# Kernel optimization log

Measured on AMD Instinct MI355X. Metric: run time of the kernel, lower is better.

## Reference

```python
import jax, jax.numpy as jnp
import numpy as np

HIDDEN = 1024
HEADS = 16
HEAD_DIM = HIDDEN // HEADS


def setup_inputs() -> dict:
    key = jax.random.key(0)
    ks = jax.random.split(key, 9)
    B, S, D = 8, 1370, HIDDEN
    x = jax.random.normal(ks[0], (B, S, D), dtype=jnp.float32)
    s = 1.0 / np.sqrt(D)
    Wq = jax.random.normal(ks[1], (D, D), dtype=jnp.float32) * s
    bq = jnp.zeros((D,), dtype=jnp.float32)
    Wk = jax.random.normal(ks[2], (D, D), dtype=jnp.float32) * s
    bk = jnp.zeros((D,), dtype=jnp.float32)
    Wv = jax.random.normal(ks[3], (D, D), dtype=jnp.float32) * s
    bv = jnp.zeros((D,), dtype=jnp.float32)
    Wo = jax.random.normal(ks[4], (D, D), dtype=jnp.float32) * s
    bo = jnp.zeros((D,), dtype=jnp.float32)
    return {"x": x, "Wq": Wq, "bq": bq, "Wk": Wk, "bk": bk,
            "Wv": Wv, "bv": bv, "Wo": Wo, "bo": bo}


def reference(x, Wq, bq, Wk, bk, Wv, bv, Wo, bo):
    B, S, D = x.shape
    H, Dh = HEADS, HEAD_DIM
    # separate Q/K/V projections
    q = (x @ Wq + bq).reshape(B, S, H, Dh).transpose(0, 2, 1, 3)  # [B,H,S,Dh]
    k = (x @ Wk + bk).reshape(B, S, H, Dh).transpose(0, 2, 1, 3)
    v = (x @ Wv + bv).reshape(B, S, H, Dh).transpose(0, 2, 1, 3)
    scale = jnp.asarray(Dh, q.dtype) ** -0.5
    attn = jnp.einsum('bhqd,bhkd->bhqk', q, k) * scale  # [B,H,S,S]
    attn = jax.nn.softmax(attn, axis=-1)
    out = jnp.einsum('bhqk,bhkd->bhqd', attn, v)        # [B,H,S,Dh]
    out = out.transpose(0, 2, 1, 3).reshape(B, S, D)
    return out @ Wo + bo
```

## Files before the change

### kernel.cpp

```cpp
#include <hip/hip_runtime.h>
#include <stdint.h>

#define DEV __device__ __forceinline__

typedef unsigned short u16;
typedef __attribute__((ext_vector_type(8))) __bf16 bf16x8;
typedef __attribute__((ext_vector_type(8))) u16 u16x8;
typedef __attribute__((ext_vector_type(4))) u16 u16x4;
typedef __attribute__((ext_vector_type(4))) float floatx4;

#define S_LEN 1370
#define S_PAD 1408
#define NH 16
#define DH 64
#define M_TOK (8 * S_LEN)
#define NKT (S_PAD / 64)
#define CEXP 0.18033688f

DEV u16 f2bf(float f) {
    union { float f; uint32_t u; } v; v.f = f;
    uint32_t u = v.u + 0x7fffu + ((v.u >> 16) & 1u);
    return (u16)(u >> 16);
}

typedef const __attribute__((address_space(1))) void as1_cvoid;
typedef __attribute__((address_space(3))) void as3_void;

DEV void async16(const void* g, void* s) {
    __builtin_amdgcn_global_load_lds((as1_cvoid*)g, (as3_void*)s, 16, 0, 0);
}

__global__ void cvt_bf16(const float* __restrict__ src, u16* __restrict__ dst) {
    const size_t i0 = ((size_t)blockIdx.x * 256 + threadIdx.x) * 8;
    const float4 a = *(const float4*)(src + i0);
    const float4 b = *(const float4*)(src + i0 + 4);
    u16x8 o;
    o[0] = f2bf(a.x); o[1] = f2bf(a.y); o[2] = f2bf(a.z); o[3] = f2bf(a.w);
    o[4] = f2bf(b.x); o[5] = f2bf(b.y); o[6] = f2bf(b.z); o[7] = f2bf(b.w);
    *(u16x8*)(dst + i0) = o;
}

__global__ void transpose4(const float* __restrict__ w0, const float* __restrict__ w1,
                           const float* __restrict__ w2, const float* __restrict__ w3,
                           u16* __restrict__ t0, u16* __restrict__ t1,
                           u16* __restrict__ t2, u16* __restrict__ t3) {
    __shared__ u16 tile[64][65];
    const float* src; u16* dst;
    switch (blockIdx.z) {
        case 0: src = w0; dst = t0; break;
        case 1: src = w1; dst = t1; break;
        case 2: src = w2; dst = t2; break;
        default: src = w3; dst = t3; break;
    }
    const int tx = blockIdx.x, ty = blockIdx.y, tid = threadIdx.x;
#pragma unroll
    for (int i = 0; i < 16; i++) {
        int e = i * 256 + tid, r = e >> 6, c = e & 63;
        tile[r][c] = f2bf(src[(size_t)(ty * 64 + r) * 1024 + tx * 64 + c]);
    }
    __syncthreads();
#pragma unroll
    for (int i = 0; i < 16; i++) {
        int e = i * 256 + tid, r = e >> 6, c = e & 63;
        dst[(size_t)(tx * 64 + r) * 1024 + ty * 64 + c] = tile[c][r];
    }
}

#define GEMM_KLOOP(M_, N_)                                                     \
    floatx4 acc[4][4];                                                         \
    _Pragma("unroll")                                                          \
    for (int i = 0; i < 4; i++)                                                \
        _Pragma("unroll")                                                      \
        for (int j = 0; j < 4; j++) acc[i][j] = (floatx4){0.f, 0.f, 0.f, 0.f}; \
    const int srow = tid >> 2;                                                 \
    const int kb = (tid & 3) * 16;                                             \
    int ar0 = mbase + srow;          if (ar0 > (M_) - 1) ar0 = (M_) - 1;       \
    int ar1 = mbase + 64 + srow;     if (ar1 > (M_) - 1) ar1 = (M_) - 1;       \
    int br0 = nbase + srow;          if (br0 > (N_) - 1) br0 = (N_) - 1;       \
    int br1 = nbase + 64 + srow;     if (br1 > (N_) - 1) br1 = (N_) - 1;       \
    const char* pA = (const char*)A;                                           \
    const char* pB = (const char*)BT;                                          \
    char* ldsA = (char*)As + w * 1024;                                         \
    char* ldsB = (char*)Bs + w * 1024;                                         \
    for (int kt = 0; kt < 32; kt++) {                                          \
        const int koff = kt * 64 + kb;                                         \
        async16(pA + (size_t)ar0 * 2048 + koff, ldsA);                         \
        async16(pA + (size_t)ar1 * 2048 + koff, ldsA + 4096);                  \
        async16(pB + (size_t)br0 * 2048 + koff, ldsB);                         \
        async16(pB + (size_t)br1 * 2048 + koff, ldsB + 4096);                  \
        __syncthreads();                                                       \
        bf16x8 af[4], bfv[4];                                                  \
        _Pragma("unroll")                                                      \
        for (int mi = 0; mi < 4; mi++)                                         \
            af[mi] = __builtin_bit_cast(bf16x8,                                \
                *(const u16x8*)&As[(wm + mi * 16 + l15) * 32 + quad * 8]);     \
        _Pragma("unroll")                                                      \
        for (int ni = 0; ni < 4; ni++)                                         \
            bfv[ni] = __builtin_bit_cast(bf16x8,                               \
                *(const u16x8*)&Bs[(wn + ni * 16 + l15) * 32 + quad * 8]);     \
        _Pragma("unroll")                                                      \
        for (int mi = 0; mi < 4; mi++)                                         \
            _Pragma("unroll")                                                  \
            for (int ni = 0; ni < 4; ni++)                                     \
                acc[mi][ni] = __builtin_amdgcn_mfma_f32_16x16x32_bf16(         \
                    af[mi], bfv[ni], acc[mi][ni], 0, 0, 0);                    \
        __syncthreads();                                                       \
    }

__global__ void gemm_qkv(const u16* __restrict__ A, const u16* __restrict__ BT,
                         const float* __restrict__ bq, const float* __restrict__ bk,
                         const float* __restrict__ bv, u16* __restrict__ Cq,
                         u16* __restrict__ Ck, u16* __restrict__ VT, int M) {
    __shared__ u16 As[128 * 32];
    __shared__ u16 Bs[128 * 32];
    const int tid = threadIdx.x;
    const int w = tid >> 6, lane = tid & 63, quad = lane >> 4, l15 = lane & 15;
    const int mbase = blockIdx.x * 128, nbase = blockIdx.y * 128;
    const int wm = (w >> 1) * 64, wn = (w & 1) * 64;

    GEMM_KLOOP(M, 3072)

    const int sel = nbase >> 10;
    if (sel == 0) {
#pragma unroll
        for (int ni = 0; ni < 4; ni++) {
            const int n = nbase + wn + ni * 16 + l15;
            const float bb = bq[n];
#pragma unroll
            for (int mi = 0; mi < 4; mi++)
#pragma unroll
                for (int r = 0; r < 4; r++) {
                    const int m = mbase + wm + mi * 16 + quad * 4 + r;
                    if (m < M) Cq[(size_t)m * 1024 + n] = f2bf((acc[mi][ni][r] + bb) * CEXP);
                }
        }
    } else if (sel == 1) {
#pragma unroll
        for (int ni = 0; ni < 4; ni++) {
            const int n = nbase - 1024 + wn + ni * 16 + l15;
            const float bb = bk[n];
#pragma unroll
            for (int mi = 0; mi < 4; mi++)
#pragma unroll
                for (int r = 0; r < 4; r++) {
                    const int m = mbase + wm + mi * 16 + quad * 4 + r;
                    if (m < M) Ck[(size_t)m * 1024 + n] = f2bf(acc[mi][ni][r] + bb);
                }
        }
    } else {
#pragma unroll
        for (int ni = 0; ni < 4; ni++) {
            const int fe = nbase - 2048 + wn + ni * 16 + l15;
            const float bb = bv[fe];
            const int hh = fe >> 6, dd = fe & 63;
#pragma unroll
            for (int mi = 0; mi < 4; mi++)
#pragma unroll
                for (int r = 0; r < 4; r++) {
                    const int m = mbase + wm + mi * 16 + quad * 4 + r;
                    if (m < M) {
                        const int btk = m / S_LEN;
                        const int ss = m - btk * S_LEN;
                        VT[(size_t)((btk * NH + hh) * DH + dd) * S_PAD + ss] =
                            f2bf(acc[mi][ni][r] + bb);
                    }
                }
        }
    }
}

__global__ void gemm_o(const u16* __restrict__ A, const u16* __restrict__ BT,
                       const float* __restrict__ bias, float* __restrict__ C, int M) {
    __shared__ u16 As[128 * 32];
    __shared__ u16 Bs[128 * 32];
    const int tid = threadIdx.x;
    const int w = tid >> 6, lane = tid & 63, quad = lane >> 4, l15 = lane & 15;
    const int mbase = blockIdx.x * 128, nbase = blockIdx.y * 128;
    const int wm = (w >> 1) * 64, wn = (w & 1) * 64;

    GEMM_KLOOP(M, 1024)

#pragma unroll
    for (int ni = 0; ni < 4; ni++) {
        const int n = nbase + wn + ni * 16 + l15;
        const float bb = bias[n];
#pragma unroll
        for (int mi = 0; mi < 4; mi++)
#pragma unroll
            for (int r = 0; r < 4; r++) {
                const int m = mbase + wm + mi * 16 + quad * 4 + r;
                if (m < M) C[(size_t)m * 1024 + n] = acc[mi][ni][r] + bb;
            }
    }
}

__global__ void flash_attn(const u16* __restrict__ Q, const u16* __restrict__ K,
                           const u16* __restrict__ VT, u16* __restrict__ O) {
    __shared__ u16 Ks[2 * 64 * 32];
    __shared__ u16 Vs[2 * 64 * 32];
    __shared__ u16 Ps[4][32 * 72];

    const int tid = threadIdx.x;
    const int w = tid >> 6, lane = tid & 63, quad = lane >> 4, l15 = lane & 15;
    const int bh = blockIdx.x, b = bh >> 4, h = bh & 15;
    const int q0 = blockIdx.y * 128 + w * 32;

    bf16x8 qf[2][2];
#pragma unroll
    for (int mi = 0; mi < 2; mi++) {
        int qr = q0 + mi * 16 + l15;
        if (qr > S_LEN - 1) qr = S_LEN - 1;
        const u16* qp = Q + (size_t)(b * S_LEN + qr) * 1024 + h * 64 + quad * 8;
        qf[mi][0] = __builtin_bit_cast(bf16x8, *(const u16x8*)qp);
        qf[mi][1] = __builtin_bit_cast(bf16x8, *(const u16x8*)(qp + 32));
    }

    floatx4 o_acc[2][4];
#pragma unroll
    for (int mi = 0; mi < 2; mi++)
#pragma unroll
        for (int nd = 0; nd < 4; nd++) o_acc[mi][nd] = (floatx4){0.f, 0.f, 0.f, 0.f};
    float lacc[2] = {0.f, 0.f};

    const int lrow = lane >> 2;
    const int scol = ((lane & 3) ^ ((lane >> 3) & 3)) * 16;
    const char* Kbl = (const char*)K + ((size_t)b * S_LEN * 1024 + h * 64) * 2 + scol;
    const char* Vbl = (const char*)VT +
                      ((size_t)(bh * 64 + w * 16 + lrow) * S_PAD) * 2 + scol;
    char* KsB = (char*)Ks;
    char* VsB = (char*)Vs;
    u16* Pw = Ps[w];

    const int rcol = (quad ^ ((l15 >> 1) & 3)) * 16;

#define STAGE(KT)                                                              \
    {                                                                          \
        int key_ = (KT) * 64 + w * 16 + lrow;                                  \
        if (key_ > S_LEN - 1) key_ = S_LEN - 1;                                \
        const char* kg_ = Kbl + (size_t)key_ * 2048;                           \
        char* kd_ = KsB + (w * 16) * 64;                                       \
        async16(kg_, kd_);                                                     \
        async16(kg_ + 64, kd_ + 4096);                                         \
        const char* vg_ = Vbl + (KT) * 128;                                    \
        char* vd_ = VsB + (w * 16) * 64;                                       \
        async16(vg_, vd_);                                                     \
        async16(vg_ + 64, vd_ + 4096);                                         \
    }

    STAGE(0)
    asm volatile("s_waitcnt vmcnt(0)" ::: "memory");
    __syncthreads();

    for (int kt = 0; kt < NKT; kt++) {
        floatx4 st[2][4];
#pragma unroll
        for (int mi = 0; mi < 2; mi++)
#pragma unroll
            for (int ni = 0; ni < 4; ni++) st[mi][ni] = (floatx4){0.f, 0.f, 0.f, 0.f};
#pragma unroll
        for (int kk = 0; kk < 2; kk++)
#pragma unroll
            for (int ni = 0; ni < 4; ni++) {
                bf16x8 kf = __builtin_bit_cast(bf16x8,
                    *(const u16x8*)(KsB + kk * 4096 + (ni * 16 + l15) * 64 + rcol));
                st[0][ni] = __builtin_amdgcn_mfma_f32_16x16x32_bf16(kf, qf[0][kk], st[0][ni], 0, 0, 0);
                st[1][ni] = __builtin_amdgcn_mfma_f32_16x16x32_bf16(kf, qf[1][kk], st[1][ni], 0, 0, 0);
            }

        if (kt == NKT - 1) {
#pragma unroll
            for (int ni = 0; ni < 4; ni++)
#pragma unroll
                for (int r = 0; r < 4; r++) {
                    const bool oob = (kt * 64 + ni * 16 + quad * 4 + r) >= S_LEN;
                    if (oob) { st[0][ni][r] = -16384.f; st[1][ni][r] = -16384.f; }
                }
        }

#pragma unroll
        for (int mi = 0; mi < 2; mi++)
#pragma unroll
            for (int ni = 0; ni < 4; ni++) {
                u16x4 pq;
#pragma unroll
                for (int r = 0; r < 4; r++) {
                    const float p = __builtin_amdgcn_exp2f(st[mi][ni][r]);
                    lacc[mi] += p;
                    union { float f; uint32_t u; } cv; cv.f = p;
                    pq[r] = (u16)((cv.u + 0x8000u) >> 16);
                }
                *(u16x4*)&Pw[(mi * 16 + l15) * 72 + ni * 16 + quad * 4] = pq;
            }

        __asm__ __volatile__("" ::: "memory");

#pragma unroll
        for (int kk = 0; kk < 2; kk++) {
            bf16x8 pf0 = __builtin_bit_cast(bf16x8,
                *(const u16x8*)&Pw[(l15) * 72 + kk * 32 + quad * 8]);
            bf16x8 pf1 = __builtin_bit_cast(bf16x8,
                *(const u16x8*)&Pw[(16 + l15) * 72 + kk * 32 + quad * 8]);
#pragma unroll
            for (int nd = 0; nd < 4; nd++) {
                bf16x8 vf = __builtin_bit_cast(bf16x8,
                    *(const u16x8*)(VsB + kk * 4096 + (nd * 16 + l15) * 64 + rcol));
                o_acc[0][nd] = __builtin_amdgcn_mfma_f32_16x16x32_bf16(pf0, vf, o_acc[0][nd], 0, 0, 0);
                o_acc[1][nd] = __builtin_amdgcn_mfma_f32_16x16x32_bf16(pf1, vf, o_acc[1][nd], 0, 0, 0);
            }
        }

        __syncthreads();
        if (kt + 1 < NKT) {
            STAGE(kt + 1)
            asm volatile("s_waitcnt vmcnt(0)" ::: "memory");
            __syncthreads();
        }
    }

    float linv[2];
#pragma unroll
    for (int mi = 0; mi < 2; mi++) {
        float rs = lacc[mi];
        rs += __shfl_xor(rs, 16);
        rs += __shfl_xor(rs, 32);
        linv[mi] = 1.f / rs;
    }

#pragma unroll
    for (int mi = 0; mi < 2; mi++)
#pragma unroll
        for (int r = 0; r < 4; r++) {
            const float inv = __shfl(linv[mi], quad * 4 + r);
            const int q = q0 + mi * 16 + quad * 4 + r;
            if (q < S_LEN) {
                u16* op = O + (size_t)(b * S_LEN + q) * 1024 + h * 64;
#pragma unroll
                for (int nd = 0; nd < 4; nd++)
                    op[nd * 16 + l15] = f2bf(o_acc[mi][nd][r] * inv);
            }
        }
}

extern "C" void kernel_launch(void* const* d_in, const int* in_sizes, int n_in,
                              void* d_out, int out_size, void* d_ws, size_t ws_size,
                              hipStream_t stream) {
    const float* x  = (const float*)d_in[0];
    const float* Wq = (const float*)d_in[1];
    const float* bq = (const float*)d_in[2];
    const float* Wk = (const float*)d_in[3];
    const float* bk = (const float*)d_in[4];
    const float* Wv = (const float*)d_in[5];
    const float* bv = (const float*)d_in[6];
    const float* Wo = (const float*)d_in[7];
    const float* bo = (const float*)d_in[8];
    float* out = (float*)d_out;

    u16* WqT = (u16*)d_ws;
    u16* WkT = WqT + (size_t)1024 * 1024;
    u16* WvT = WkT + (size_t)1024 * 1024;
    u16* WoT = WvT + (size_t)1024 * 1024;
    u16* xb  = WoT + (size_t)1024 * 1024;
    u16* Qb  = xb + (size_t)M_TOK * 1024;
    u16* Kb  = Qb + (size_t)M_TOK * 1024;
    u16* VTb = Kb + (size_t)M_TOK * 1024;
    u16* Ob  = VTb + (size_t)128 * 64 * S_PAD;

    cvt_bf16<<<dim3(M_TOK * 1024 / 2048), 256, 0, stream>>>(x, xb);
    transpose4<<<dim3(16, 16, 4), 256, 0, stream>>>(Wq, Wk, Wv, Wo, WqT, WkT, WvT, WoT);
    gemm_qkv<<<dim3(86, 24), 256, 0, stream>>>(xb, WqT, bq, bk, bv, Qb, Kb, VTb, M_TOK);
    flash_attn<<<dim3(128, 11), 256, 0, stream>>>(Qb, Kb, VTb, Ob);
    gemm_o<<<dim3(86, 8), 256, 0, stream>>>(Ob, WoT, bo, out, M_TOK);
}
```

Baseline: 364.5 us.

## Double-buffer K/V tiles in flash attention and swizzle GEMM LDS reads

The attention kernel now keeps two LDS buffers for K and V. The next tile's async load is issued at the top of each iteration and overlaps the current tile's QK and PV MFMA work, replacing the old pattern of loading, waiting on vmcnt(0) and hitting a second barrier. The GEMM k-loop also XOR-swizzles which 16-byte column chunk each lane fetches, and reads with the matching swizzle, to cut LDS bank conflicts on fragment loads. The cost is doubled K/V LDS footprint in attention, which may lower occupancy, and the code now relies on __syncthreads to drain the outstanding async loads.

```diff
diff --git a/kernel.cpp b/kernel.cpp
--- a/kernel.cpp
+++ b/kernel.cpp
@@ -73,7 +73,8 @@
         _Pragma("unroll")                                                      \
         for (int j = 0; j < 4; j++) acc[i][j] = (floatx4){0.f, 0.f, 0.f, 0.f}; \
     const int srow = tid >> 2;                                                 \
-    const int kb = (tid & 3) * 16;                                             \
+    const int kb = ((tid & 3) ^ ((tid >> 3) & 3)) * 16;     \
+    const int rsw = (quad ^ ((l15 >> 1) & 3)) * 8;          \
     int ar0 = mbase + srow;          if (ar0 > (M_) - 1) ar0 = (M_) - 1;       \
     int ar1 = mbase + 64 + srow;     if (ar1 > (M_) - 1) ar1 = (M_) - 1;       \
     int br0 = nbase + srow;          if (br0 > (N_) - 1) br0 = (N_) - 1;       \
@@ -93,11 +94,11 @@
         _Pragma("unroll")                                                      \
         for (int mi = 0; mi < 4; mi++)                                         \
             af[mi] = __builtin_bit_cast(bf16x8,                                \
-                *(const u16x8*)&As[(wm + mi * 16 + l15) * 32 + quad * 8]);     \
+                *(const u16x8*)&As[(wm + mi * 16 + l15) * 32 + rsw]);          \
         _Pragma("unroll")                                                      \
         for (int ni = 0; ni < 4; ni++)                                         \
             bfv[ni] = __builtin_bit_cast(bf16x8,                               \
-                *(const u16x8*)&Bs[(wn + ni * 16 + l15) * 32 + quad * 8]);     \
+                *(const u16x8*)&Bs[(wn + ni * 16 + l15) * 32 + rsw]);          \
         _Pragma("unroll")                                                      \
         for (int mi = 0; mi < 4; mi++)                                         \
             _Pragma("unroll")                                                  \
@@ -196,8 +197,8 @@
 
 __global__ void flash_attn(const u16* __restrict__ Q, const u16* __restrict__ K,
                            const u16* __restrict__ VT, u16* __restrict__ O) {
-    __shared__ u16 Ks[2 * 64 * 32];
-    __shared__ u16 Vs[2 * 64 * 32];
+    __shared__ u16 Ks[2][2 * 64 * 32];
+    __shared__ u16 Vs[2][2 * 64 * 32];
     __shared__ u16 Ps[4][32 * 72];
 
     const int tid = threadIdx.x;
@@ -233,25 +234,29 @@
 
     const int rcol = (quad ^ ((l15 >> 1) & 3)) * 16;
 
-#define STAGE(KT)                                                              \
+#define STAGE(KT, BI)                                                          \
     {                                                                          \
         int key_ = (KT) * 64 + w * 16 + lrow;                                  \
         if (key_ > S_LEN - 1) key_ = S_LEN - 1;                                \
         const char* kg_ = Kbl + (size_t)key_ * 2048;                           \
-        char* kd_ = KsB + (w * 16) * 64;                                       \
+        char* kd_ = KsB + (BI) * 8192 + (w * 16) * 64;                         \
         async16(kg_, kd_);                                                     \
         async16(kg_ + 64, kd_ + 4096);                                         \
         const char* vg_ = Vbl + (KT) * 128;                                    \
-        char* vd_ = VsB + (w * 16) * 64;                                       \
+        char* vd_ = VsB + (BI) * 8192 + (w * 16) * 64;                         \
         async16(vg_, vd_);                                                     \
         async16(vg_ + 64, vd_ + 4096);                                         \
     }
 
-    STAGE(0)
-    asm volatile("s_waitcnt vmcnt(0)" ::: "memory");
+    STAGE(0, 0)
     __syncthreads();
 
     for (int kt = 0; kt < NKT; kt++) {
+        const int bi = kt & 1;
+        if (kt + 1 < NKT) STAGE(kt + 1, bi ^ 1)
+        const char* KsT = KsB + bi * 8192;
+        const char* VsT = VsB + bi * 8192;
+
         floatx4 st[2][4];
 #pragma unroll
         for (int mi = 0; mi < 2; mi++)
@@ -262,7 +267,7 @@
 #pragma unroll
             for (int ni = 0; ni < 4; ni++) {
                 bf16x8 kf = __builtin_bit_cast(bf16x8,
-                    *(const u16x8*)(KsB + kk * 4096 + (ni * 16 + l15) * 64 + rcol));
+                    *(const u16x8*)(KsT + kk * 4096 + (ni * 16 + l15) * 64 + rcol));
                 st[0][ni] = __builtin_amdgcn_mfma_f32_16x16x32_bf16(kf, qf[0][kk], st[0][ni], 0, 0, 0);
                 st[1][ni] = __builtin_amdgcn_mfma_f32_16x16x32_bf16(kf, qf[1][kk], st[1][ni], 0, 0, 0);
             }
@@ -303,18 +308,12 @@
 #pragma unroll
             for (int nd = 0; nd < 4; nd++) {
                 bf16x8 vf = __builtin_bit_cast(bf16x8,
-                    *(const u16x8*)(VsB + kk * 4096 + (nd * 16 + l15) * 64 + rcol));
+                    *(const u16x8*)(VsT + kk * 4096 + (nd * 16 + l15) * 64 + rcol));
                 o_acc[0][nd] = __builtin_amdgcn_mfma_f32_16x16x32_bf16(pf0, vf, o_acc[0][nd], 0, 0, 0);
                 o_acc[1][nd] = __builtin_amdgcn_mfma_f32_16x16x32_bf16(pf1, vf, o_acc[1][nd], 0, 0, 0);
             }
         }
-
         __syncthreads();
-        if (kt + 1 < NKT) {
-            STAGE(kt + 1)
-            asm volatile("s_waitcnt vmcnt(0)" ::: "memory");
-            __syncthreads();
-        }
     }
 
     float linv[2];
```

Result: slower. 378.9 us (+4.0%).
